# Performance work log

Hardware: AMD Instinct MI355X
Metric: run time of the kernel (lower is better)

Reference implementation:

```python
import jax, jax.numpy as jnp
import numpy as np

Q_OFFSET = 128  # stored quants are in [0,255); subtract to get signed int8 range


def setup_inputs() -> dict:
    key = jax.random.key(0)
    k1, k2, k3, k4 = jax.random.split(key, 4)
    O, NB, BS = 4096, 128, 32  # out_features, num_blocks, block_size (Q8_0)
    x = jax.random.normal(k1, (4, 1024, NB * BS), dtype=jnp.float16)
    q_weight = jax.random.randint(k2, (O, NB, BS), 0, 255, dtype=jnp.int32)
    scales = jax.random.uniform(k3, (O, NB), dtype=jnp.float16) * jnp.float16(0.05)
    bias = jax.random.normal(k4, (O,), dtype=jnp.float16)
    return {"x": x, "q_weight": q_weight, "scales": scales, "bias": bias}


def reference(x, q_weight, scales, bias):
    # GGUF Q8_0-style on-the-fly dequant: w[o, b*32+j] = (q[o,b,j]-128) * scale[o,b]
    q = q_weight.astype(jnp.float16) - jnp.float16(Q_OFFSET)  # [O, NB, BS]
    w = (q * scales[:, :, None]).reshape(scales.shape[0], -1)  # [O, I]
    # linear: y = x @ w^T + bias
    return jnp.einsum('bsi,oi->bso', x, w) + bias
```

## Files before the change

### kernel.cpp

```cpp
#include <hip/hip_runtime.h>
#include <stdint.h>


#define QOFF 128

typedef __bf16 bf16_t;
typedef __bf16 bf16x8 __attribute__((ext_vector_type(8)));
typedef float f32x4 __attribute__((ext_vector_type(4)));

#define WAIT_VM6_LGKM0 0x0076
#define WAIT_VM0_LGKM0 0x0070

__global__ __launch_bounds__(256) void prep_kernel(
    const int* __restrict__ q, const float* __restrict__ scales,
    const float* __restrict__ X, bf16_t* __restrict__ W,
    bf16_t* __restrict__ Xb, int K, int NB, int nDeq) {
  const int b = blockIdx.x;
  if (b < nDeq) {
    const size_t e = ((size_t)b * 256 + threadIdx.x) * 8;
    const int o = (int)(e / (size_t)K);
    const int i = (int)(e % (size_t)K);
    const float s = scales[o * NB + (i >> 5)];
    int4 a = *(const int4*)(q + e);
    int4 c = *(const int4*)(q + e + 4);
    const int* av = (const int*)&a;
    const int* cv = (const int*)&c;
    bf16x8 t;
#pragma unroll
    for (int j = 0; j < 4; ++j) t[j] = (bf16_t)((float)(av[j] - QOFF) * s);
#pragma unroll
    for (int j = 0; j < 4; ++j) t[4 + j] = (bf16_t)((float)(cv[j] - QOFF) * s);
    *(bf16x8*)(W + e) = t;
  } else {
    const size_t e = ((size_t)(b - nDeq) * 256 + threadIdx.x) * 8;
    float4 a = *(const float4*)(X + e);
    float4 c = *(const float4*)(X + e + 4);
    bf16x8 t;
    t[0] = (bf16_t)a.x; t[1] = (bf16_t)a.y; t[2] = (bf16_t)a.z; t[3] = (bf16_t)a.w;
    t[4] = (bf16_t)c.x; t[5] = (bf16_t)c.y; t[6] = (bf16_t)c.z; t[7] = (bf16_t)c.w;
    *(bf16x8*)(Xb + e) = t;
  }
}

__device__ __forceinline__ void async16(bf16_t* lds, const bf16_t* g) {
  __builtin_amdgcn_global_load_lds(
      (const __attribute__((address_space(1))) unsigned int*)(const void*)g,
      (__attribute__((address_space(3))) unsigned int*)(void*)lds, 16, 0, 0);
}

__global__ __launch_bounds__(256, 2) void gemm_pipe2(
    const bf16_t* __restrict__ A,
    const bf16_t* __restrict__ B,
    const float* __restrict__ bias,
    float* __restrict__ C,
    int M, int N, int K) {
  __shared__ bf16_t lsA[3][128 * 32];
  __shared__ bf16_t lsB[3][256 * 32];

  const int tid = threadIdx.x;
  const int lane = tid & 63;
  const int wave = tid >> 6;
  const int m0 = blockIdx.y * 128;
  const int n0 = blockIdx.x * 256;
  const int wm = (wave >> 1) * 64;
  const int wn = (wave & 1) * 128;
  const int r = lane & 15;
  const int qd = lane >> 4;

  f32x4 acc[4][8] = {};

  const int ea0 = tid * 8;
  const int ea1 = 2048 + tid * 8;
  const bf16_t* gA0 = A + (size_t)(m0 + (ea0 >> 5)) * K + (ea0 & 31);
  const bf16_t* gA1 = A + (size_t)(m0 + (ea1 >> 5)) * K + (ea1 & 31);
  const bf16_t* gB0 = B + (size_t)(n0 + (ea0 >> 5)) * K + (ea0 & 31);
  const bf16_t* gB1 = B + (size_t)(n0 + (ea1 >> 5)) * K + (ea1 & 31);
  const bf16_t* gB2 = B + (size_t)(n0 + 128 + (ea0 >> 5)) * K + (ea0 & 31);
  const bf16_t* gB3 = B + (size_t)(n0 + 128 + (ea1 >> 5)) * K + (ea1 & 31);

  auto issue = [&](int s, int koff) {
    async16(&lsA[s][ea0], gA0 + koff);
    async16(&lsA[s][ea1], gA1 + koff);
    async16(&lsB[s][ea0], gB0 + koff);
    async16(&lsB[s][ea1], gB1 + koff);
    async16(&lsB[s][4096 + ea0], gB2 + koff);
    async16(&lsB[s][4096 + ea1], gB3 + koff);
  };
  auto compute = [&](int s) {
    bf16x8 af[4], bfv[8];
#pragma unroll
    for (int i = 0; i < 4; ++i)
      af[i] = *(const bf16x8*)&lsA[s][(wm + i * 16 + r) * 32 + qd * 8];
#pragma unroll
    for (int j = 0; j < 8; ++j)
      bfv[j] = *(const bf16x8*)&lsB[s][(wn + j * 16 + r) * 32 + qd * 8];
#pragma unroll
    for (int mi = 0; mi < 4; ++mi)
#pragma unroll
      for (int ni = 0; ni < 8; ++ni)
        acc[mi][ni] = __builtin_amdgcn_mfma_f32_16x16x32_bf16(
            af[mi], bfv[ni], acc[mi][ni], 0, 0, 0);
  };

  const int ITERS = K / 32;

  issue(0, 0);
  issue(1, 32);
  __builtin_amdgcn_s_waitcnt(WAIT_VM6_LGKM0);
  __builtin_amdgcn_s_barrier();

  int k = 0;
  const int steady = (ITERS - 2) / 3;
  for (int j = 0; j < steady; ++j) {
#pragma unroll
    for (int u = 0; u < 3; ++u) {
      issue((u + 2) % 3, (k + 2) * 32);
      compute(u);
      __builtin_amdgcn_s_waitcnt(WAIT_VM6_LGKM0);
      __builtin_amdgcn_s_barrier();
      ++k;
    }
  }
  compute(0);
  __builtin_amdgcn_s_waitcnt(WAIT_VM0_LGKM0);
  __builtin_amdgcn_s_barrier();
  compute(1);

#pragma unroll
  for (int ni = 0; ni < 8; ++ni) {
    const int n = n0 + wn + ni * 16 + r;
    const float bv = bias[n];
#pragma unroll
    for (int mi = 0; mi < 4; ++mi) {
      const int mbase = m0 + wm + mi * 16 + qd * 4;
#pragma unroll
      for (int reg = 0; reg < 4; ++reg) {
        C[(size_t)(mbase + reg) * N + n] = acc[mi][ni][reg] + bv;
      }
    }
  }
}

__global__ __launch_bounds__(256) void gemm_db(
    const bf16_t* __restrict__ A, const bf16_t* __restrict__ B,
    const float* __restrict__ bias, float* __restrict__ C, int M, int N,
    int K) {
  __shared__ bf16_t lsA[2][128 * 32];
  __shared__ bf16_t lsB[2][128 * 32];

  const int tid = threadIdx.x;
  const int lane = tid & 63;
  const int wave = tid >> 6;
  const int m0 = blockIdx.y * 128;
  const int n0 = blockIdx.x * 128;
  const int wm = (wave >> 1) * 64;
  const int wn = (wave & 1) * 64;
  const int r = lane & 15;
  const int qd = lane >> 4;

  f32x4 acc[4][4] = {};

  const int e0 = tid * 8;
  const int e1 = 2048 + tid * 8;
  const bf16_t* gA0 = A + (size_t)(m0 + (e0 >> 5)) * K + (e0 & 31);
  const bf16_t* gA1 = A + (size_t)(m0 + (e1 >> 5)) * K + (e1 & 31);
  const bf16_t* gB0 = B + (size_t)(n0 + (e0 >> 5)) * K + (e0 & 31);
  const bf16_t* gB1 = B + (size_t)(n0 + (e1 >> 5)) * K + (e1 & 31);

  async16(&lsA[0][e0], gA0);
  async16(&lsA[0][e1], gA1);
  async16(&lsB[0][e0], gB0);
  async16(&lsB[0][e1], gB1);

  int buf = 0;
  for (int k0 = 0; k0 < K; k0 += 32, buf ^= 1) {
    __syncthreads();
    if (k0 + 32 < K) {
      const int nk = k0 + 32;
      async16(&lsA[buf ^ 1][e0], gA0 + nk);
      async16(&lsA[buf ^ 1][e1], gA1 + nk);
      async16(&lsB[buf ^ 1][e0], gB0 + nk);
      async16(&lsB[buf ^ 1][e1], gB1 + nk);
    }
    bf16x8 af[4], bfv[4];
#pragma unroll
    for (int i = 0; i < 4; ++i) {
      af[i] = *(const bf16x8*)&lsA[buf][(wm + i * 16 + r) * 32 + qd * 8];
      bfv[i] = *(const bf16x8*)&lsB[buf][(wn + i * 16 + r) * 32 + qd * 8];
    }
#pragma unroll
    for (int mi = 0; mi < 4; ++mi)
#pragma unroll
      for (int ni = 0; ni < 4; ++ni)
        acc[mi][ni] = __builtin_amdgcn_mfma_f32_16x16x32_bf16(
            af[mi], bfv[ni], acc[mi][ni], 0, 0, 0);
  }

#pragma unroll
  for (int ni = 0; ni < 4; ++ni) {
    const int n = n0 + wn + ni * 16 + r;
    const float bv = bias[n];
#pragma unroll
    for (int mi = 0; mi < 4; ++mi) {
      const int mbase = m0 + wm + mi * 16 + qd * 4;
#pragma unroll
      for (int reg = 0; reg < 4; ++reg) {
        C[(size_t)(mbase + reg) * N + n] = acc[mi][ni][reg] + bv;
      }
    }
  }
}

__global__ __launch_bounds__(256) void gemm_fused(
    const float* __restrict__ Af, const int* __restrict__ q,
    const float* __restrict__ scales, const float* __restrict__ bias,
    float* __restrict__ C, int M, int N, int K, int NB) {
  __shared__ bf16_t lsA[128 * 32];
  __shared__ bf16_t lsB[128 * 32];

  const int tid = threadIdx.x;
  const int lane = tid & 63;
  const int wave = tid >> 6;
  const int m0 = blockIdx.y * 128;
  const int n0 = blockIdx.x * 128;
  const int wm = (wave >> 1) * 64;
  const int wn = (wave & 1) * 64;
  const int r = lane & 15;
  const int qd = lane >> 4;

  const int e = tid * 16;
  const int row = e >> 5;
  const int col = e & 31;

  const float* gAf = Af + (size_t)(m0 + row) * K + col;
  const int* gQ = q + (size_t)(n0 + row) * K + col;
  const float* gS = scales + (size_t)(n0 + row) * NB;

  f32x4 acc[4][4] = {};

  for (int k0 = 0; k0 < K; k0 += 32) {
    bf16x8 a0, a1, b0, b1;
    {
      float4 f0 = *(const float4*)(gAf + k0);
      float4 f1 = *(const float4*)(gAf + k0 + 4);
      float4 f2 = *(const float4*)(gAf + k0 + 8);
      float4 f3 = *(const float4*)(gAf + k0 + 12);
      a0[0] = (bf16_t)f0.x; a0[1] = (bf16_t)f0.y; a0[2] = (bf16_t)f0.z; a0[3] = (bf16_t)f0.w;
      a0[4] = (bf16_t)f1.x; a0[5] = (bf16_t)f1.y; a0[6] = (bf16_t)f1.z; a0[7] = (bf16_t)f1.w;
      a1[0] = (bf16_t)f2.x; a1[1] = (bf16_t)f2.y; a1[2] = (bf16_t)f2.z; a1[3] = (bf16_t)f2.w;
      a1[4] = (bf16_t)f3.x; a1[5] = (bf16_t)f3.y; a1[6] = (bf16_t)f3.z; a1[7] = (bf16_t)f3.w;
    }
    {
      const float s = gS[k0 >> 5];
      int qv[16];
      *(int4*)&qv[0] = *(const int4*)(gQ + k0);
      *(int4*)&qv[4] = *(const int4*)(gQ + k0 + 4);
      *(int4*)&qv[8] = *(const int4*)(gQ + k0 + 8);
      *(int4*)&qv[12] = *(const int4*)(gQ + k0 + 12);
#pragma unroll
      for (int j = 0; j < 8; ++j) b0[j] = (bf16_t)((float)(qv[j] - QOFF) * s);
#pragma unroll
      for (int j = 0; j < 8; ++j)
        b1[j] = (bf16_t)((float)(qv[8 + j] - QOFF) * s);
    }

    __syncthreads();
    *(bf16x8*)&lsA[e] = a0;
    *(bf16x8*)&lsA[e + 8] = a1;
    *(bf16x8*)&lsB[e] = b0;
    *(bf16x8*)&lsB[e + 8] = b1;
    __syncthreads();

    bf16x8 af[4], bfv[4];
#pragma unroll
    for (int i = 0; i < 4; ++i) {
      af[i] = *(const bf16x8*)&lsA[(wm + i * 16 + r) * 32 + qd * 8];
      bfv[i] = *(const bf16x8*)&lsB[(wn + i * 16 + r) * 32 + qd * 8];
    }
#pragma unroll
    for (int mi = 0; mi < 4; ++mi)
#pragma unroll
      for (int ni = 0; ni < 4; ++ni)
        acc[mi][ni] = __builtin_amdgcn_mfma_f32_16x16x32_bf16(
            af[mi], bfv[ni], acc[mi][ni], 0, 0, 0);
  }

#pragma unroll
  for (int ni = 0; ni < 4; ++ni) {
    const int n = n0 + wn + ni * 16 + r;
    const float bv = bias[n];
#pragma unroll
    for (int mi = 0; mi < 4; ++mi) {
      const int mbase = m0 + wm + mi * 16 + qd * 4;
#pragma unroll
      for (int reg = 0; reg < 4; ++reg) {
        C[(size_t)(mbase + reg) * N + n] = acc[mi][ni][reg] + bv;
      }
    }
  }
}

extern "C" void kernel_launch(void* const* d_in, const int* in_sizes, int n_in,
                              void* d_out, int out_size, void* d_ws,
                              size_t ws_size, hipStream_t stream) {
  const float* x = (const float*)d_in[0];
  const int* qw = (const int*)d_in[1];
  const float* scales = (const float*)d_in[2];
  const float* bias = (const float*)d_in[3];
  float* out = (float*)d_out;

  const int O = in_sizes[3];
  const int K = in_sizes[1] / O;
  const int NB = in_sizes[2] / O;
  const int M = in_sizes[0] / K;
  (void)n_in; (void)out_size;

  const size_t Wbytes = (size_t)O * K * sizeof(bf16_t);
  const size_t Xbytes = (size_t)M * K * sizeof(bf16_t);

  if (ws_size >= Wbytes + Xbytes) {
    bf16_t* W = (bf16_t*)d_ws;
    bf16_t* Xb = (bf16_t*)((char*)d_ws + Wbytes);
    const int nDeq = (int)((size_t)O * K / 2048);
    const int nCvt = (int)((size_t)M * K / 2048);
    prep_kernel<<<nDeq + nCvt, 256, 0, stream>>>(qw, scales, x, W, Xb, K, NB,
                                                 nDeq);
    const int iters = K / 32;
    if (iters >= 5 && (iters - 2) % 3 == 0 && (M % 128) == 0 &&
        (O % 256) == 0) {
      dim3 grid(O / 256, M / 128);
      gemm_pipe2<<<grid, 256, 0, stream>>>(Xb, W, bias, out, M, O, K);
    } else {
      dim3 grid(O / 128, M / 128);
      gemm_db<<<grid, 256, 0, stream>>>(Xb, W, bias, out, M, O, K);
    }
  } else {
    dim3 grid(O / 128, M / 128);
    gemm_fused<<<grid, 256, 0, stream>>>(x, qw, scales, bias, out, M, O, K,
                                         NB);
  }
}
```

Baseline: 304.4 us.

## Replace GEMM with 256x256 8-wave ping-pong kernel using swizzled LDS

Replaces the 128x256 triple-buffered GEMM with a 512-thread kernel computing 256x256 tiles and K-steps of 64. It uses double-buffered, XOR-swizzled LDS and splits each tile into four quadrant MFMA blocks, interleaving the async global-to-LDS loads between them. It also raises wave priority around the MFMA blocks and remaps workgroup IDs across groups of 8 for better cache locality. This increases per-block reuse and overlaps loads with compute, at the cost of many extra barriers, a large LDS footprint, and high register pressure from a 32-tile accumulator per wave.

```diff
diff --git a/kernel.cpp b/kernel.cpp
--- a/kernel.cpp
+++ b/kernel.cpp
@@ -8,8 +8,9 @@
 typedef __bf16 bf16x8 __attribute__((ext_vector_type(8)));
 typedef float f32x4 __attribute__((ext_vector_type(4)));
 
-#define WAIT_VM6_LGKM0 0x0076
-#define WAIT_VM0_LGKM0 0x0070
+#define W_LGKM0 0xC07F
+#define W_VM4 0x0F74
+#define W_VM0 0x0F70
 
 __global__ __launch_bounds__(256) void prep_kernel(
     const int* __restrict__ q, const float* __restrict__ scales,
@@ -48,90 +49,171 @@
       (__attribute__((address_space(3))) unsigned int*)(void*)lds, 16, 0, 0);
 }
 
-__global__ __launch_bounds__(256, 2) void gemm_pipe2(
+template <int QM, int QN>
+__device__ __forceinline__ void mm_block(f32x4 (&acc)[8][4],
+                                         const bf16x8 (&af)[4][2],
+                                         const bf16x8 (&bv)[2][2]) {
+  __builtin_amdgcn_s_setprio(1);
+#pragma unroll
+  for (int ks = 0; ks < 2; ++ks)
+#pragma unroll
+    for (int fi = 0; fi < 4; ++fi)
+#pragma unroll
+      for (int fj = 0; fj < 2; ++fj)
+        acc[QM * 4 + fi][QN * 2 + fj] = __builtin_amdgcn_mfma_f32_16x16x32_bf16(
+            af[fi][ks], bv[fj][ks], acc[QM * 4 + fi][QN * 2 + fj], 0, 0, 0);
+  __builtin_amdgcn_s_setprio(0);
+}
+
+__device__ __forceinline__ void rd_a(const bf16_t* base, const int* swz,
+                                     bf16x8 (&af)[4][2]) {
+#pragma unroll
+  for (int fi = 0; fi < 4; ++fi)
+#pragma unroll
+    for (int ks = 0; ks < 2; ++ks)
+      af[fi][ks] = *(const bf16x8*)(base + fi * 1024 + swz[ks]);
+}
+
+__device__ __forceinline__ void rd_b(const bf16_t* base, const int* swz,
+                                     bf16x8 (&bv)[2][2]) {
+#pragma unroll
+  for (int fj = 0; fj < 2; ++fj)
+#pragma unroll
+    for (int ks = 0; ks < 2; ++ks)
+      bv[fj][ks] = *(const bf16x8*)(base + fj * 1024 + swz[ks]);
+}
+
+__global__ __launch_bounds__(512, 2) void gemm_8ph(
     const bf16_t* __restrict__ A,
     const bf16_t* __restrict__ B,
     const float* __restrict__ bias,
     float* __restrict__ C,
     int M, int N, int K) {
-  __shared__ bf16_t lsA[3][128 * 32];
-  __shared__ bf16_t lsB[3][256 * 32];
+  __shared__ bf16_t lsA[2][256 * 64];
+  __shared__ bf16_t lsB[2][256 * 64];
 
   const int tid = threadIdx.x;
   const int lane = tid & 63;
   const int wave = tid >> 6;
-  const int m0 = blockIdx.y * 128;
-  const int n0 = blockIdx.x * 256;
-  const int wm = (wave >> 1) * 64;
-  const int wn = (wave & 1) * 128;
   const int r = lane & 15;
   const int qd = lane >> 4;
-
-  f32x4 acc[4][8] = {};
-
-  const int ea0 = tid * 8;
-  const int ea1 = 2048 + tid * 8;
-  const bf16_t* gA0 = A + (size_t)(m0 + (ea0 >> 5)) * K + (ea0 & 31);
-  const bf16_t* gA1 = A + (size_t)(m0 + (ea1 >> 5)) * K + (ea1 & 31);
-  const bf16_t* gB0 = B + (size_t)(n0 + (ea0 >> 5)) * K + (ea0 & 31);
-  const bf16_t* gB1 = B + (size_t)(n0 + (ea1 >> 5)) * K + (ea1 & 31);
-  const bf16_t* gB2 = B + (size_t)(n0 + 128 + (ea0 >> 5)) * K + (ea0 & 31);
-  const bf16_t* gB3 = B + (size_t)(n0 + 128 + (ea1 >> 5)) * K + (ea1 & 31);
-
-  auto issue = [&](int s, int koff) {
-    async16(&lsA[s][ea0], gA0 + koff);
-    async16(&lsA[s][ea1], gA1 + koff);
-    async16(&lsB[s][ea0], gB0 + koff);
-    async16(&lsB[s][ea1], gB1 + koff);
-    async16(&lsB[s][4096 + ea0], gB2 + koff);
-    async16(&lsB[s][4096 + ea1], gB3 + koff);
+  const int wm = (wave >> 2) * 128;
+  const int wn = (wave & 3) * 64;
+
+  const int nbx = N >> 8;
+  const int nwg = gridDim.x;
+  int wg = blockIdx.x;
+  if ((nwg & 7) == 0) wg = (wg & 7) * (nwg >> 3) + (wg >> 3);
+  const int m0 = (wg / nbx) * 256;
+  const int n0 = (wg % nbx) * 256;
+
+  f32x4 acc[8][4] = {};
+
+  const int srow = tid >> 3;
+  const int sslot = (tid & 7) ^ (srow & 7);
+  const bf16_t* gA0 = A + (size_t)(m0 + srow) * K + sslot * 8;
+  const bf16_t* gB0 = B + (size_t)(n0 + srow) * K + sslot * 8;
+
+  auto stgA = [&](bf16_t* dstTile, int half, int koff) {
+    bf16_t* d = dstTile + half * 8192 + tid * 8;
+    const bf16_t* g = gA0 + (size_t)(half * 128) * K + koff;
+    async16(d, g);
+    async16(d + 4096, g + 64 * (size_t)K);
   };
-  auto compute = [&](int s) {
-    bf16x8 af[4], bfv[8];
-#pragma unroll
-    for (int i = 0; i < 4; ++i)
-      af[i] = *(const bf16x8*)&lsA[s][(wm + i * 16 + r) * 32 + qd * 8];
-#pragma unroll
-    for (int j = 0; j < 8; ++j)
-      bfv[j] = *(const bf16x8*)&lsB[s][(wn + j * 16 + r) * 32 + qd * 8];
-#pragma unroll
-    for (int mi = 0; mi < 4; ++mi)
-#pragma unroll
-      for (int ni = 0; ni < 8; ++ni)
-        acc[mi][ni] = __builtin_amdgcn_mfma_f32_16x16x32_bf16(
-            af[mi], bfv[ni], acc[mi][ni], 0, 0, 0);
+  auto stgB = [&](bf16_t* dstTile, int half, int koff) {
+    bf16_t* d = dstTile + half * 8192 + tid * 8;
+    const bf16_t* g = gB0 + (size_t)(half * 128) * K + koff;
+    async16(d, g);
+    async16(d + 4096, g + 64 * (size_t)K);
   };
 
-  const int ITERS = K / 32;
-
-  issue(0, 0);
-  issue(1, 32);
-  __builtin_amdgcn_s_waitcnt(WAIT_VM6_LGKM0);
+  const int swz[2] = {(qd ^ (r & 7)) * 8, ((4 + qd) ^ (r & 7)) * 8};
+  const bf16_t* a0base = &lsA[0][(wm + r) * 64];
+  const bf16_t* a1base = &lsA[1][(wm + r) * 64];
+  const bf16_t* b0base = &lsB[0][(wn + r) * 64];
+  const bf16_t* b1base = &lsB[1][(wn + r) * 64];
+
+  const int NT = K >> 6;
+  const int NITER = NT >> 1;
+
+  stgA(lsA[0], 0, 0);
+  stgA(lsA[0], 1, 0);
+  stgB(lsB[0], 0, 0);
+  stgB(lsB[0], 1, 0);
+  stgB(lsB[1], 0, 64);
+  stgB(lsB[1], 1, 64);
+  __builtin_amdgcn_s_waitcnt(W_VM4);
   __builtin_amdgcn_s_barrier();
 
-  int k = 0;
-  const int steady = (ITERS - 2) / 3;
-  for (int j = 0; j < steady; ++j) {
-#pragma unroll
-    for (int u = 0; u < 3; ++u) {
-      issue((u + 2) % 3, (k + 2) * 32);
-      compute(u);
-      __builtin_amdgcn_s_waitcnt(WAIT_VM6_LGKM0);
-      __builtin_amdgcn_s_barrier();
-      ++k;
-    }
-  }
-  compute(0);
-  __builtin_amdgcn_s_waitcnt(WAIT_VM0_LGKM0);
-  __builtin_amdgcn_s_barrier();
-  compute(1);
-
-#pragma unroll
-  for (int ni = 0; ni < 8; ++ni) {
+  bf16x8 af[4][2], bf0[2][2], bf1[2][2];
+
+#pragma unroll 1
+  for (int j = 0; j < NITER; ++j) {
+    const int k1 = (2 * j + 1) * 64;
+    int t2 = 2 * j + 2; if (t2 >= NT) t2 -= NT;
+    int t3 = 2 * j + 3; if (t3 >= NT) t3 -= NT;
+    const int k2 = t2 * 64;
+    const int k3 = t3 * 64;
+
+    rd_a(a0base, swz, af);
+    rd_b(b0base, swz, bf0);
+    stgA(lsA[1], 0, k1);
+    __builtin_amdgcn_s_barrier();
+    __builtin_amdgcn_s_waitcnt(W_LGKM0);
+    mm_block<0, 0>(acc, af, bf0);
+    __builtin_amdgcn_s_barrier();
+    rd_b(b0base + 2048, swz, bf1);
+    stgA(lsA[1], 1, k1);
+    __builtin_amdgcn_s_barrier();
+    __builtin_amdgcn_s_waitcnt(W_LGKM0);
+    mm_block<0, 1>(acc, af, bf1);
+    __builtin_amdgcn_s_barrier();
+    rd_a(a0base + 4096, swz, af);
+    stgB(lsB[0], 0, k2);
+    __builtin_amdgcn_s_barrier();
+    __builtin_amdgcn_s_waitcnt(W_LGKM0);
+    mm_block<1, 1>(acc, af, bf1);
+    __builtin_amdgcn_s_barrier();
+    stgB(lsB[0], 1, k2);
+    __builtin_amdgcn_s_barrier();
+    mm_block<1, 0>(acc, af, bf0);
+    __builtin_amdgcn_s_waitcnt(W_VM4);
+    __builtin_amdgcn_s_barrier();
+
+    rd_a(a1base, swz, af);
+    rd_b(b1base, swz, bf0);
+    stgA(lsA[0], 0, k2);
+    __builtin_amdgcn_s_barrier();
+    __builtin_amdgcn_s_waitcnt(W_LGKM0);
+    mm_block<0, 0>(acc, af, bf0);
+    __builtin_amdgcn_s_barrier();
+    rd_b(b1base + 2048, swz, bf1);
+    stgA(lsA[0], 1, k2);
+    __builtin_amdgcn_s_barrier();
+    __builtin_amdgcn_s_waitcnt(W_LGKM0);
+    mm_block<0, 1>(acc, af, bf1);
+    __builtin_amdgcn_s_barrier();
+    rd_a(a1base + 4096, swz, af);
+    stgB(lsB[1], 0, k3);
+    __builtin_amdgcn_s_barrier();
+    __builtin_amdgcn_s_waitcnt(W_LGKM0);
+    mm_block<1, 1>(acc, af, bf1);
+    __builtin_amdgcn_s_barrier();
+    stgB(lsB[1], 1, k3);
+    __builtin_amdgcn_s_barrier();
+    mm_block<1, 0>(acc, af, bf0);
+    __builtin_amdgcn_s_waitcnt(W_VM4);
+    __builtin_amdgcn_s_barrier();
+  }
+
+  __builtin_amdgcn_s_waitcnt(W_VM0);
+
+#pragma unroll
+  for (int ni = 0; ni < 4; ++ni) {
     const int n = n0 + wn + ni * 16 + r;
     const float bv = bias[n];
 #pragma unroll
-    for (int mi = 0; mi < 4; ++mi) {
+    for (int mi = 0; mi < 8; ++mi) {
       const int mbase = m0 + wm + mi * 16 + qd * 4;
 #pragma unroll
       for (int reg = 0; reg < 4; ++reg) {
@@ -325,11 +407,9 @@
     const int nCvt = (int)((size_t)M * K / 2048);
     prep_kernel<<<nDeq + nCvt, 256, 0, stream>>>(qw, scales, x, W, Xb, K, NB,
                                                  nDeq);
-    const int iters = K / 32;
-    if (iters >= 5 && (iters - 2) % 3 == 0 && (M % 128) == 0 &&
-        (O % 256) == 0) {
-      dim3 grid(O / 256, M / 128);
-      gemm_pipe2<<<grid, 256, 0, stream>>>(Xb, W, bias, out, M, O, K);
+    if ((M % 256) == 0 && (O % 256) == 0 && (K % 128) == 0) {
+      const int nwg = (M / 256) * (O / 256);
+      gemm_8ph<<<nwg, 512, 0, stream>>>(Xb, W, bias, out, M, O, K);
     } else {
       dim3 grid(O / 128, M / 128);
       gemm_db<<<grid, 256, 0, stream>>>(Xb, W, bias, out, M, O, K);
```

New measurement: 298.5 us. Within noise of the previous version (-1.9%).
